# Kernel tuning notes

Measured on AMD Instinct MI355X. Metric: run time of the kernel, lower is better.

## Reference

```python
import jax, jax.numpy as jnp
import numpy as np

DIM = 128
IND_DIM = 5
HEADS = 4
DIM_HEAD = 32
HIDDEN = HEADS * DIM_HEAD  # 128
SCALE = DIM_HEAD ** -0.5


def setup_inputs() -> dict:
    key = jax.random.key(0)
    ks = jax.random.split(key, 6)
    b, n = 1, 512
    x = jax.random.normal(ks[0], (b, DIM, n), dtype=jnp.float32)
    indicator = jax.random.normal(ks[1], (b, IND_DIM, n, n), dtype=jnp.float32)
    # conv1d kernels with kernel_size=1 are just (out, in) matrices
    w_qkv = jax.random.normal(ks[2], (HIDDEN * 3, DIM), dtype=jnp.float32) * (DIM ** -0.5)
    w_ind = jax.random.normal(ks[3], (HIDDEN * 2, IND_DIM), dtype=jnp.float32) * (IND_DIM ** -0.5)
    w_out = jax.random.normal(ks[4], (DIM, HIDDEN), dtype=jnp.float32) * (HIDDEN ** -0.5)
    b_out = jax.random.normal(ks[5], (DIM,), dtype=jnp.float32) * 0.01
    return {"x": x, "indicator": indicator, "w_qkv": w_qkv,
            "w_ind": w_ind, "w_out": w_out, "b_out": b_out}


def reference(x, indicator, w_qkv, w_ind, w_out, b_out):
    b, c, n = x.shape
    h, dh = HEADS, DIM_HEAD
    # pointwise conv = channel matmul
    qkv = jnp.einsum('oc,bcn->bon', w_qkv, x)  # (b, 3*hidden, n)
    q, k, v = jnp.split(qkv, 3, axis=1)
    q = q.reshape(b, h, dh, n)
    k = k.reshape(b, h, dh, n)
    v = v.reshape(b, h, dh, n)
    ind = jnp.einsum('oc,bcij->boij', w_ind, indicator)  # (b, 2*hidden, n, n)
    ind_q, ind_k = jnp.split(ind, 2, axis=1)
    ind_q = ind_q.reshape(b, h, dh, n, n)
    ind_k = ind_k.reshape(b, h, dh, n, n)
    qq = (q[..., :, None] + ind_q) * SCALE        # (b, h, dh, n, n)
    kk = k[..., None, :] + ind_k                   # (b, h, dh, n, n)
    sim = jnp.einsum('bhdij,bhdij->bhij', qq, kk)  # (b, h, n, n)
    attn = jax.nn.softmax(sim, axis=-1)
    out = jnp.einsum('bhij,bhdj->bhdi', attn, v)   # (b, h, dh, n)
    out = out.reshape(b, h * dh, n)
    return jnp.einsum('oc,bcn->bon', w_out, out) + b_out[None, :, None]
```

## Files before the change

### kernel.cpp

```cpp
#include <hip/hip_runtime.h>
#include <math.h>

#define N      512
#define DIMC   128
#define HEADS  4
#define DH     32
#define INDC   5
#define SCALE  0.1767766952966369f

#define QKV_ROWS 384
#define AQ_BASE  384
#define AK_BASE  404
#define TOT_ROWS 424

__global__ __launch_bounds__(256) void pre_kernel(const float* __restrict__ w_qkv,
                                                  const float* __restrict__ w_ind,
                                                  const float* __restrict__ x,
                                                  float* __restrict__ rows_out,
                                                  float* __restrict__ Mh) {
    const int bx = blockIdx.x;
    const int t  = threadIdx.x;
    if (bx == TOT_ROWS / 4) {
        if (blockIdx.y != 0) return;
        if (t < HEADS * INDC * INDC) {
            const int h = t / 25, c = (t / 5) % 5, cc = t % 5;
            float acc = 0.f;
            for (int d = 0; d < DH; ++d)
                acc = fmaf(w_ind[(h * DH + d) * INDC + c],
                           w_ind[(DIMC + h * DH + d) * INDC + cc], acc);
            Mh[t] = acc;
        }
        return;
    }
    __shared__ float ws[4 * DIMC];
    const int o0 = bx * 4;
    for (int idx = t; idx < 4 * DIMC; idx += 256) {
        const int rl = idx >> 7, m = idx & 127;
        const int row = o0 + rl;
        float val;
        if (row < QKV_ROWS) {
            val = w_qkv[row * DIMC + m];
        } else if (row < AK_BASE) {
            const int r = row - AQ_BASE, h = r / INDC, c = r % INDC;
            float acc = 0.f;
            for (int d = 0; d < DH; ++d)
                acc = fmaf(w_qkv[(h * DH + d) * DIMC + m],
                           w_ind[(DIMC + h * DH + d) * INDC + c], acc);
            val = acc;
        } else {
            const int r = row - AK_BASE, h = r / INDC, c = r % INDC;
            float acc = 0.f;
            for (int d = 0; d < DH; ++d)
                acc = fmaf(w_qkv[(DIMC + h * DH + d) * DIMC + m],
                           w_ind[(h * DH + d) * INDC + c], acc);
            val = acc;
        }
        ws[idx] = val;
    }
    __syncthreads();
    const int i = blockIdx.y * 256 + t;
    float acc[4] = {0.f, 0.f, 0.f, 0.f};
#pragma unroll 4
    for (int c = 0; c < DIMC; ++c) {
        const float xv = x[c * N + i];
#pragma unroll
        for (int r = 0; r < 4; ++r) acc[r] = fmaf(ws[r * DIMC + c], xv, acc[r]);
    }
#pragma unroll
    for (int r = 0; r < 4; ++r) rows_out[(o0 + r) * N + i] = acc[r];
}

__global__ __launch_bounds__(256) void attn_kernel(const float* __restrict__ rows,
                                                   const float* __restrict__ ind,
                                                   const float* __restrict__ Mh,
                                                   float* __restrict__ att_out) {
    const int i    = blockIdx.x;
    const int h    = blockIdx.y;
    const int t    = threadIdx.x;
    const int lane = t & 63;
    const int wave = t >> 6;

    __shared__ float qs[DH];
    __shared__ float aqs[INDC];
    __shared__ float ms[INDC * INDC];
    __shared__ float ps[N];
    __shared__ float red[4];

    const float* q  = rows;
    const float* k  = rows + DIMC * N;
    const float* v  = rows + 2 * DIMC * N;
    const float* Aq = rows + 3 * DIMC * N;
    const float* Ak = Aq + HEADS * INDC * N;

    if (t < DH) qs[t] = q[(h * DH + t) * N + i];
    else if (t >= 64 && t < 64 + INDC) aqs[t - 64] = Aq[(h * INDC + (t - 64)) * N + i];
    else if (t >= 128 && t < 128 + INDC * INDC) ms[t - 128] = Mh[h * 25 + (t - 128)];
    __syncthreads();

    float2 ic[INDC];
#pragma unroll
    for (int c = 0; c < INDC; ++c)
        ic[c] = ((const float2*)(ind + (c * N + i) * N))[t];

    float2 qk = {0.f, 0.f};
#pragma unroll
    for (int d = 0; d < DH; ++d) {
        const float2 kv = ((const float2*)(k + (h * DH + d) * N))[t];
        qk.x = fmaf(qs[d], kv.x, qk.x);
        qk.y = fmaf(qs[d], kv.y, qk.y);
    }
    float2 lin = {0.f, 0.f};
#pragma unroll
    for (int c = 0; c < INDC; ++c) {
        const float2 akv = ((const float2*)(Ak + (h * INDC + c) * N))[t];
        lin.x = fmaf(aqs[c] + akv.x, ic[c].x, lin.x);
        lin.y = fmaf(aqs[c] + akv.y, ic[c].y, lin.y);
    }
    float2 quad = {0.f, 0.f};
#pragma unroll
    for (int c = 0; c < INDC; ++c) {
        float2 tc = {0.f, 0.f};
#pragma unroll
        for (int cc = 0; cc < INDC; ++cc) {
            const float mv = ms[c * INDC + cc];
            tc.x = fmaf(mv, ic[cc].x, tc.x);
            tc.y = fmaf(mv, ic[cc].y, tc.y);
        }
        quad.x = fmaf(ic[c].x, tc.x, quad.x);
        quad.y = fmaf(ic[c].y, tc.y, quad.y);
    }
    const float s0 = SCALE * (qk.x + lin.x + quad.x);
    const float s1 = SCALE * (qk.y + lin.y + quad.y);

    float m = fmaxf(s0, s1);
#pragma unroll
    for (int off = 32; off; off >>= 1) m = fmaxf(m, __shfl_down(m, off, 64));
    if (lane == 0) red[wave] = m;
    __syncthreads();
    m = fmaxf(fmaxf(red[0], red[1]), fmaxf(red[2], red[3]));
    const float e0 = __expf(s0 - m);
    const float e1 = __expf(s1 - m);
    float sum = e0 + e1;
#pragma unroll
    for (int off = 32; off; off >>= 1) sum += __shfl_down(sum, off, 64);
    __syncthreads();
    if (lane == 0) red[wave] = sum;
    __syncthreads();
    sum = (red[0] + red[1]) + (red[2] + red[3]);
    const float rs = 1.f / sum;
    ((float2*)ps)[t] = make_float2(e0 * rs, e1 * rs);
    __syncthreads();

    const float2* ps2 = (const float2*)ps;
#pragma unroll
    for (int dd = 0; dd < 8; ++dd) {
        const int d = wave * 8 + dd;
        const float2* vr = (const float2*)(v + (h * DH + d) * N);
        float acc = 0.f;
#pragma unroll
        for (int s = 0; s < 4; ++s) {
            const float2 p  = ps2[lane + 64 * s];
            const float2 vv = vr[lane + 64 * s];
            acc = fmaf(p.x, vv.x, fmaf(p.y, vv.y, acc));
        }
#pragma unroll
        for (int off = 32; off; off >>= 1) acc += __shfl_down(acc, off, 64);
        if (lane == 0) att_out[(h * DH + d) * N + i] = acc;
    }
}

__global__ __launch_bounds__(256) void outproj_kernel(const float* __restrict__ w,
                                                      const float* __restrict__ b,
                                                      const float* __restrict__ att,
                                                      float* __restrict__ out) {
    __shared__ float ws[4 * DIMC];
    const int o0 = blockIdx.x * 4;
    const int t  = threadIdx.x;
    for (int idx = t; idx < 4 * DIMC; idx += 256) ws[idx] = w[o0 * DIMC + idx];
    __syncthreads();
    const int i = blockIdx.y * 256 + t;
    float acc[4] = {0.f, 0.f, 0.f, 0.f};
#pragma unroll 4
    for (int c = 0; c < DIMC; ++c) {
        const float av = att[c * N + i];
#pragma unroll
        for (int r = 0; r < 4; ++r) acc[r] = fmaf(ws[r * DIMC + c], av, acc[r]);
    }
#pragma unroll
    for (int r = 0; r < 4; ++r) out[(o0 + r) * N + i] = acc[r] + b[o0 + r];
}

extern "C" void kernel_launch(void* const* d_in, const int* in_sizes, int n_in,
                              void* d_out, int out_size, void* d_ws, size_t ws_size,
                              hipStream_t stream) {
    const float* x         = (const float*)d_in[0];
    const float* indicator = (const float*)d_in[1];
    const float* w_qkv     = (const float*)d_in[2];
    const float* w_ind     = (const float*)d_in[3];
    const float* w_out     = (const float*)d_in[4];
    const float* b_out     = (const float*)d_in[5];
    float* out = (float*)d_out;

    float* rows = (float*)d_ws;
    float* Mh   = rows + TOT_ROWS * N;
    float* att  = Mh + 128;

    pre_kernel<<<dim3(TOT_ROWS / 4 + 1, 2), 256, 0, stream>>>(w_qkv, w_ind, x, rows, Mh);
    attn_kernel<<<dim3(N, HEADS), 256, 0, stream>>>(rows, indicator, Mh, att);
    outproj_kernel<<<dim3(DIMC / 4, 2), 256, 0, stream>>>(w_out, b_out, att, out);
}
```

Measured before the change: 118.5 us.

## Fuse all heads and output projection into one attention block per query

The attention kernel now handles all four heads for each query row in a single block, so the indicator tile is loaded once per query instead of once per head. The quadratic indicator term uses a symmetrised 15-term form. The output projection is folded into the attention kernel using a transposed w_out written by the pre-kernel, and the pre-kernel now processes two columns per thread with float4 weight reads. This drops one launch and the repeated indicator reads, at the cost of fewer blocks (512), more registers, and a large shared-memory reduction buffer that may lower occupancy.

Result: no change. 117.4 us (-1.0%).

```diff
diff --git a/kernel.cpp b/kernel.cpp
--- a/kernel.cpp
+++ b/kernel.cpp
@@ -12,79 +12,109 @@
 #define AQ_BASE  384
 #define AK_BASE  404
 #define TOT_ROWS 424
+#define NROW_BLK (TOT_ROWS / 4)
+
+#define ROWS_F   0
+#define MHS_F    (TOT_ROWS * N)
+#define WOUTT_F  (MHS_F + 64)
 
 __global__ __launch_bounds__(256) void pre_kernel(const float* __restrict__ w_qkv,
                                                   const float* __restrict__ w_ind,
                                                   const float* __restrict__ x,
-                                                  float* __restrict__ rows_out,
-                                                  float* __restrict__ Mh) {
+                                                  const float* __restrict__ w_out,
+                                                  float* __restrict__ ws) {
     const int bx = blockIdx.x;
     const int t  = threadIdx.x;
-    if (bx == TOT_ROWS / 4) {
-        if (blockIdx.y != 0) return;
+    float* rows   = ws + ROWS_F;
+    float* MhS    = ws + MHS_F;
+    float* w_outT = ws + WOUTT_F;
+
+    if (bx == NROW_BLK) {
+        __shared__ float mraw[HEADS * INDC * INDC];
         if (t < HEADS * INDC * INDC) {
             const int h = t / 25, c = (t / 5) % 5, cc = t % 5;
             float acc = 0.f;
             for (int d = 0; d < DH; ++d)
                 acc = fmaf(w_ind[(h * DH + d) * INDC + c],
                            w_ind[(DIMC + h * DH + d) * INDC + cc], acc);
-            Mh[t] = acc;
+            mraw[t] = acc;
+        }
+        __syncthreads();
+        if (t < 64) {
+            const int h = t >> 4, idx = t & 15;
+            const int PC[10]  = {0, 0, 0, 0, 1, 1, 1, 2, 2, 3};
+            const int PCC[10] = {1, 2, 3, 4, 2, 3, 4, 3, 4, 4};
+            float s = 0.f;
+            if (idx < 5) {
+                s = mraw[h * 25 + idx * 5 + idx];
+            } else if (idx < 15) {
+                const int c = PC[idx - 5], cc = PCC[idx - 5];
+                s = mraw[h * 25 + c * 5 + cc] + mraw[h * 25 + cc * 5 + c];
+            }
+            MhS[h * 16 + idx] = s;
+        }
+        for (int idx = t; idx < DIMC * DIMC; idx += 256) {
+            const int o = idx >> 7, c = idx & 127;
+            w_outT[c * DIMC + o] = w_out[idx];
         }
         return;
     }
-    __shared__ float ws[4 * DIMC];
+
+    __shared__ float ws2[4 * DIMC];
     const int o0 = bx * 4;
     for (int idx = t; idx < 4 * DIMC; idx += 256) {
-        const int rl = idx >> 7, m = idx & 127;
-        const int row = o0 + rl;
+        const int r = idx & 3, m = idx >> 2;
+        const int row = o0 + r;
         float val;
         if (row < QKV_ROWS) {
             val = w_qkv[row * DIMC + m];
         } else if (row < AK_BASE) {
-            const int r = row - AQ_BASE, h = r / INDC, c = r % INDC;
+            const int rr = row - AQ_BASE, h = rr / INDC, c = rr % INDC;
             float acc = 0.f;
             for (int d = 0; d < DH; ++d)
                 acc = fmaf(w_qkv[(h * DH + d) * DIMC + m],
                            w_ind[(DIMC + h * DH + d) * INDC + c], acc);
             val = acc;
         } else {
-            const int r = row - AK_BASE, h = r / INDC, c = r % INDC;
+            const int rr = row - AK_BASE, h = rr / INDC, c = rr % INDC;
             float acc = 0.f;
             for (int d = 0; d < DH; ++d)
                 acc = fmaf(w_qkv[(DIMC + h * DH + d) * DIMC + m],
                            w_ind[(h * DH + d) * INDC + c], acc);
             val = acc;
         }
-        ws[idx] = val;
-    }
-    __syncthreads();
-    const int i = blockIdx.y * 256 + t;
-    float acc[4] = {0.f, 0.f, 0.f, 0.f};
-#pragma unroll 4
+        ws2[m * 4 + r] = val;
+    }
+    __syncthreads();
+
+    const float2* x2 = (const float2*)x;
+    float2 acc[4] = {{0.f,0.f},{0.f,0.f},{0.f,0.f},{0.f,0.f}};
+#pragma unroll 8
     for (int c = 0; c < DIMC; ++c) {
-        const float xv = x[c * N + i];
-#pragma unroll
-        for (int r = 0; r < 4; ++r) acc[r] = fmaf(ws[r * DIMC + c], xv, acc[r]);
-    }
-#pragma unroll
-    for (int r = 0; r < 4; ++r) rows_out[(o0 + r) * N + i] = acc[r];
+        const float2 xv = x2[c * 256 + t];
+        const float4 wv = *(const float4*)(ws2 + c * 4);
+        acc[0].x = fmaf(wv.x, xv.x, acc[0].x); acc[0].y = fmaf(wv.x, xv.y, acc[0].y);
+        acc[1].x = fmaf(wv.y, xv.x, acc[1].x); acc[1].y = fmaf(wv.y, xv.y, acc[1].y);
+        acc[2].x = fmaf(wv.z, xv.x, acc[2].x); acc[2].y = fmaf(wv.z, xv.y, acc[2].y);
+        acc[3].x = fmaf(wv.w, xv.x, acc[3].x); acc[3].y = fmaf(wv.w, xv.y, acc[3].y);
+    }
+#pragma unroll
+    for (int r = 0; r < 4; ++r)
+        ((float2*)(rows + (o0 + r) * N))[t] = acc[r];
 }
 
-__global__ __launch_bounds__(256) void attn_kernel(const float* __restrict__ rows,
+__global__ __launch_bounds__(256) void attn_kernel(const float* __restrict__ ws,
                                                    const float* __restrict__ ind,
-                                                   const float* __restrict__ Mh,
-                                                   float* __restrict__ att_out) {
+                                                   const float* __restrict__ b_out,
+                                                   float* __restrict__ out) {
     const int i    = blockIdx.x;
-    const int h    = blockIdx.y;
     const int t    = threadIdx.x;
     const int lane = t & 63;
     const int wave = t >> 6;
 
-    __shared__ float qs[DH];
-    __shared__ float aqs[INDC];
-    __shared__ float ms[INDC * INDC];
-    __shared__ float ps[N];
-    __shared__ float red[4];
+    const float* rows   = ws + ROWS_F;
+    const float* MhS    = ws + MHS_F;
+    const float* w_outT = ws + WOUTT_F;
 
     const float* q  = rows;
     const float* k  = rows + DIMC * N;
@@ -92,9 +122,18 @@
     const float* Aq = rows + 3 * DIMC * N;
     const float* Ak = Aq + HEADS * INDC * N;
 
-    if (t < DH) qs[t] = q[(h * DH + t) * N + i];
-    else if (t >= 64 && t < 64 + INDC) aqs[t - 64] = Aq[(h * INDC + (t - 64)) * N + i];
-    else if (t >= 128 && t < 128 + INDC * INDC) ms[t - 128] = Mh[h * 25 + (t - 128)];
+    __shared__ float qs[DIMC];
+    __shared__ float aqs[HEADS * INDC];
+    __shared__ float msS[HEADS * 16];
+    __shared__ float ps[HEADS][N];
+    __shared__ float red[HEADS][DH][64];
+    __shared__ float red4[2][HEADS][4];
+    __shared__ float attv[DIMC];
+    __shared__ float outred[4][DIMC];
+
+    if (t < DIMC) qs[t] = q[t * N + i];
+    else if (t >= 128 && t < 128 + HEADS * INDC) aqs[t - 128] = Aq[(t - 128) * N + i];
+    else if (t >= 160 && t < 160 + HEADS * 16) msS[t - 160] = MhS[t - 160];
     __syncthreads();
 
     float2 ic[INDC];
@@ -102,92 +141,130 @@
     for (int c = 0; c < INDC; ++c)
         ic[c] = ((const float2*)(ind + (c * N + i) * N))[t];
 
-    float2 qk = {0.f, 0.f};
-#pragma unroll
-    for (int d = 0; d < DH; ++d) {
-        const float2 kv = ((const float2*)(k + (h * DH + d) * N))[t];
-        qk.x = fmaf(qs[d], kv.x, qk.x);
-        qk.y = fmaf(qs[d], kv.y, qk.y);
-    }
-    float2 lin = {0.f, 0.f};
-#pragma unroll
-    for (int c = 0; c < INDC; ++c) {
-        const float2 akv = ((const float2*)(Ak + (h * INDC + c) * N))[t];
-        lin.x = fmaf(aqs[c] + akv.x, ic[c].x, lin.x);
-        lin.y = fmaf(aqs[c] + akv.y, ic[c].y, lin.y);
-    }
-    float2 quad = {0.f, 0.f};
-#pragma unroll
-    for (int c = 0; c < INDC; ++c) {
-        float2 tc = {0.f, 0.f};
-#pragma unroll
-        for (int cc = 0; cc < INDC; ++cc) {
-            const float mv = ms[c * INDC + cc];
-            tc.x = fmaf(mv, ic[cc].x, tc.x);
-            tc.y = fmaf(mv, ic[cc].y, tc.y);
-        }
-        quad.x = fmaf(ic[c].x, tc.x, quad.x);
-        quad.y = fmaf(ic[c].y, tc.y, quad.y);
-    }
-    const float s0 = SCALE * (qk.x + lin.x + quad.x);
-    const float s1 = SCALE * (qk.y + lin.y + quad.y);
-
-    float m = fmaxf(s0, s1);
-#pragma unroll
-    for (int off = 32; off; off >>= 1) m = fmaxf(m, __shfl_down(m, off, 64));
-    if (lane == 0) red[wave] = m;
-    __syncthreads();
-    m = fmaxf(fmaxf(red[0], red[1]), fmaxf(red[2], red[3]));
-    const float e0 = __expf(s0 - m);
-    const float e1 = __expf(s1 - m);
-    float sum = e0 + e1;
-#pragma unroll
-    for (int off = 32; off; off >>= 1) sum += __shfl_down(sum, off, 64);
-    __syncthreads();
-    if (lane == 0) red[wave] = sum;
-    __syncthreads();
-    sum = (red[0] + red[1]) + (red[2] + red[3]);
-    const float rs = 1.f / sum;
-    ((float2*)ps)[t] = make_float2(e0 * rs, e1 * rs);
-    __syncthreads();
-
-    const float2* ps2 = (const float2*)ps;
-#pragma unroll
-    for (int dd = 0; dd < 8; ++dd) {
-        const int d = wave * 8 + dd;
-        const float2* vr = (const float2*)(v + (h * DH + d) * N);
-        float acc = 0.f;
-#pragma unroll
+    float2 prod[15];
+#pragma unroll
+    for (int c = 0; c < INDC; ++c)
+        prod[c] = make_float2(ic[c].x * ic[c].x, ic[c].y * ic[c].y);
+    {
+        int p = 5;
+#pragma unroll
+        for (int c = 0; c < INDC; ++c)
+#pragma unroll
+            for (int cc = c + 1; cc < INDC; ++cc, ++p)
+                prod[p] = make_float2(ic[c].x * ic[cc].x, ic[c].y * ic[cc].y);
+    }
+
+    const float2* k2  = (const float2*)k;
+    const float2* Ak2 = (const float2*)Ak;
+    float2 sim[HEADS];
+#pragma unroll
+    for (int h = 0; h < HEADS; ++h) {
+        float2 qk = {0.f, 0.f};
+#pragma unroll
+        for (int d4 = 0; d4 < DH / 4; ++d4) {
+            const float4 qv = *(const float4*)(qs + h * DH + 4 * d4);
+            float2 kv;
+            kv = k2[(h * DH + 4 * d4 + 0) * 256 + t];
+            qk.x = fmaf(qv.x, kv.x, qk.x); qk.y = fmaf(qv.x, kv.y, qk.y);
+            kv = k2[(h * DH + 4 * d4 + 1) * 256 + t];
+            qk.x = fmaf(qv.y, kv.x, qk.x); qk.y = fmaf(qv.y, kv.y, qk.y);
+            kv = k2[(h * DH + 4 * d4 + 2) * 256 + t];
+            qk.x = fmaf(qv.z, kv.x, qk.x); qk.y = fmaf(qv.z, kv.y, qk.y);
+            kv = k2[(h * DH + 4 * d4 + 3) * 256 + t];
+            qk.x = fmaf(qv.w, kv.x, qk.x); qk.y = fmaf(qv.w, kv.y, qk.y);
+        }
+        float2 lin = {0.f, 0.f};
+#pragma unroll
+        for (int c = 0; c < INDC; ++c) {
+            const float2 akv = Ak2[(h * INDC + c) * 256 + t];
+            const float aqv = aqs[h * INDC + c];
+            lin.x = fmaf(aqv + akv.x, ic[c].x, lin.x);
+            lin.y = fmaf(aqv + akv.y, ic[c].y, lin.y);
+        }
+        float2 quad = {0.f, 0.f};
+#pragma unroll
+        for (int p = 0; p < 15; ++p) {
+            const float sv = msS[h * 16 + p];
+            quad.x = fmaf(sv, prod[p].x, quad.x);
+            quad.y = fmaf(sv, prod[p].y, quad.y);
+        }
+        sim[h].x = SCALE * (qk.x + lin.x + quad.x);
+        sim[h].y = SCALE * (qk.y + lin.y + quad.y);
+    }
+
+#pragma unroll
+    for (int h = 0; h < HEADS; ++h) {
+        float m = fmaxf(sim[h].x, sim[h].y);
+#pragma unroll
+        for (int off = 32; off; off >>= 1) m = fmaxf(m, __shfl_down(m, off, 64));
+        if (lane == 0) red4[0][h][wave] = m;
+    }
+    __syncthreads();
+    float2 e[HEADS];
+#pragma unroll
+    for (int h = 0; h < HEADS; ++h) {
+        const float m = fmaxf(fmaxf(red4[0][h][0], red4[0][h][1]),
+                              fmaxf(red4[0][h][2], red4[0][h][3]));
+        e[h].x = __expf(sim[h].x - m);
+        e[h].y = __expf(sim[h].y - m);
+        float s = e[h].x + e[h].y;
+#pragma unroll
+        for (int off = 32; off; off >>= 1) s += __shfl_down(s, off, 64);
+        if (lane == 0) red4[1][h][wave] = s;
+    }
+    __syncthreads();
+#pragma unroll
+    for (int h = 0; h < HEADS; ++h) {
+        const float s = (red4[1][h][0] + red4[1][h][1]) + (red4[1][h][2] + red4[1][h][3]);
+        const float rs = 1.f / s;
+        ((float2*)&ps[h][0])[t] = make_float2(e[h].x * rs, e[h].y * rs);
+    }
+    __syncthreads();
+
+    {
+        const int h = wave;
+        float acc[DH];
+#pragma unroll
+        for (int d = 0; d < DH; ++d) acc[d] = 0.f;
+        const float2* ps2 = (const float2*)&ps[h][0];
+        const float2* v2  = (const float2*)v;
         for (int s = 0; s < 4; ++s) {
-            const float2 p  = ps2[lane + 64 * s];
-            const float2 vv = vr[lane + 64 * s];
-            acc = fmaf(p.x, vv.x, fmaf(p.y, vv.y, acc));
-        }
-#pragma unroll
-        for (int off = 32; off; off >>= 1) acc += __shfl_down(acc, off, 64);
-        if (lane == 0) att_out[(h * DH + d) * N + i] = acc;
-    }
-}
-
-__global__ __launch_bounds__(256) void outproj_kernel(const float* __restrict__ w,
-                                                      const float* __restrict__ b,
-                                                      const float* __restrict__ att,
-                                                      float* __restrict__ out) {
-    __shared__ float ws[4 * DIMC];
-    const int o0 = blockIdx.x * 4;
-    const int t  = threadIdx.x;
-    for (int idx = t; idx < 4 * DIMC; idx += 256) ws[idx] = w[o0 * DIMC + idx];
-    __syncthreads();
-    const int i = blockIdx.y * 256 + t;
-    float acc[4] = {0.f, 0.f, 0.f, 0.f};
-#pragma unroll 4
-    for (int c = 0; c < DIMC; ++c) {
-        const float av = att[c * N + i];
-#pragma unroll
-        for (int r = 0; r < 4; ++r) acc[r] = fmaf(ws[r * DIMC + c], av, acc[r]);
-    }
-#pragma unroll
-    for (int r = 0; r < 4; ++r) out[(o0 + r) * N + i] = acc[r] + b[o0 + r];
+            const float2 p = ps2[lane + 64 * s];
+#pragma unroll
+            for (int d = 0; d < DH; ++d) {
+                const float2 vv = v2[(h * DH + d) * 256 + lane + 64 * s];
+                acc[d] = fmaf(p.x, vv.x, fmaf(p.y, vv.y, acc[d]));
+            }
+        }
+#pragma unroll
+        for (int d = 0; d < DH; ++d) red[h][d][lane ^ d] = acc[d];
+        const int d = lane & 31, half = lane >> 5;
+        float s = 0.f;
+#pragma unroll
+        for (int kk = 0; kk < 32; ++kk) s += red[h][d][(half * 32 + kk) ^ d];
+        s += __shfl_down(s, 32, 64);
+        if (lane < 32) attv[h * DH + d] = s;
+    }
+    __syncthreads();
+
+    {
+        const int po = t & 63;
+        const int quarter = t >> 6;
+        const float2* wT2 = (const float2*)w_outT;
+        float2 acc2 = {0.f, 0.f};
+#pragma unroll 8
+        for (int c = quarter * 32; c < quarter * 32 + 32; ++c) {
+            const float av = attv[c];
+            const float2 wv = wT2[c * 64 + po];
+            acc2.x = fmaf(wv.x, av, acc2.x);
+            acc2.y = fmaf(wv.y, av, acc2.y);
+        }
+        ((float2*)&outred[quarter][0])[po] = acc2;
+    }
+    __syncthreads();
+    if (t < DIMC)
+        out[t * N + i] = ((outred[0][t] + outred[1][t]) + (outred[2][t] + outred[3][t]))
+                         + b_out[t];
 }
 
 extern "C" void kernel_launch(void* const* d_in, const int* in_sizes, int n_in,
@@ -200,12 +277,8 @@
     const float* w_out     = (const float*)d_in[4];
     const float* b_out     = (const float*)d_in[5];
     float* out = (float*)d_out;
-
-    float* rows = (float*)d_ws;
-    float* Mh   = rows + TOT_ROWS * N;
-    float* att  = Mh + 128;
-
-    pre_kernel<<<dim3(TOT_ROWS / 4 + 1, 2), 256, 0, stream>>>(w_qkv, w_ind, x, rows, Mh);
-    attn_kernel<<<dim3(N, HEADS), 256, 0, stream>>>(rows, indicator, Mh, att);
-    outproj_kernel<<<dim3(DIMC / 4, 2), 256, 0, stream>>>(w_out, b_out, att, out);
+    float* ws  = (float*)d_ws;
+
+    pre_kernel<<<NROW_BLK + 1, 256, 0, stream>>>(w_qkv, w_ind, x, w_out, ws);
+    attn_kernel<<<N, 256, 0, stream>>>(ws, indicator, b_out, out);
 }
```
